# Kernel tuning notes

Hardware: AMD Instinct MI355X
Metric: run time of the kernel (lower is better)

## Reference

```python
import jax, jax.numpy as jnp
import numpy as np

B, ISIZE, HSIZE = 256, 256, 512
CLIPVAL = 2.0

def _linear(x, W, b):
    # torch nn.Linear: y = x @ W.T + b, W is [out, in]
    return x @ W.T + b

def setup_inputs() -> dict:
    key = jax.random.key(0)
    ks = jax.random.split(key, 24)
    d = {}
    d['inputs'] = jax.random.normal(ks[0], (B, ISIZE), jnp.float32)
    d['h0'] = jax.random.normal(ks[1], (B, HSIZE), jnp.float32) * 0.1
    d['c0'] = jax.random.normal(ks[2], (B, HSIZE), jnp.float32) * 0.1
    d['hebb'] = jax.random.normal(ks[3], (B, HSIZE, HSIZE), jnp.float32) * 0.01
    d['w'] = 0.02 * jax.random.uniform(ks[4], (HSIZE, HSIZE), jnp.float32) - 0.01
    d['alpha'] = 0.0001 * jax.random.uniform(ks[5], (1, 1, HSIZE), jnp.float32)
    scale_h = 1.0 / np.sqrt(HSIZE)
    scale_i = 1.0 / np.sqrt(ISIZE)
    d['h2f_w'] = jax.random.uniform(ks[6], (HSIZE, HSIZE), jnp.float32, -scale_h, scale_h)
    d['h2f_b'] = jax.random.uniform(ks[7], (HSIZE,), jnp.float32, -scale_h, scale_h)
    d['h2i_w'] = jax.random.uniform(ks[8], (HSIZE, HSIZE), jnp.float32, -scale_h, scale_h)
    d['h2i_b'] = jax.random.uniform(ks[9], (HSIZE,), jnp.float32, -scale_h, scale_h)
    d['h2opt_w'] = jax.random.uniform(ks[10], (HSIZE, HSIZE), jnp.float32, -scale_h, scale_h)
    d['h2opt_b'] = jax.random.uniform(ks[11], (HSIZE,), jnp.float32, -scale_h, scale_h)
    d['x2f_w'] = jax.random.uniform(ks[12], (HSIZE, ISIZE), jnp.float32, -scale_i, scale_i)
    d['x2f_b'] = jax.random.uniform(ks[13], (HSIZE,), jnp.float32, -scale_i, scale_i)
    d['x2i_w'] = jax.random.uniform(ks[14], (HSIZE, ISIZE), jnp.float32, -scale_i, scale_i)
    d['x2i_b'] = jax.random.uniform(ks[15], (HSIZE,), jnp.float32, -scale_i, scale_i)
    d['x2opt_w'] = jax.random.uniform(ks[16], (HSIZE, ISIZE), jnp.float32, -scale_i, scale_i)
    d['x2opt_b'] = jax.random.uniform(ks[17], (HSIZE,), jnp.float32, -scale_i, scale_i)
    d['x2c_w'] = jax.random.uniform(ks[18], (HSIZE, ISIZE), jnp.float32, -scale_i, scale_i)
    d['x2c_b'] = jax.random.uniform(ks[19], (HSIZE,), jnp.float32, -scale_i, scale_i)
    d['h2mod_w'] = jax.random.uniform(ks[20], (1, HSIZE), jnp.float32, -scale_h, scale_h)
    d['h2mod_b'] = jax.random.uniform(ks[21], (1,), jnp.float32, -scale_h, scale_h)
    d['modfanout_w'] = jax.random.uniform(ks[22], (HSIZE, 1), jnp.float32, -1.0, 1.0)
    d['modfanout_b'] = jax.random.uniform(ks[23], (HSIZE,), jnp.float32, -1.0, 1.0)
    return d

def reference(inputs, h0, c0, hebb, w, alpha,
              h2f_w, h2f_b, h2i_w, h2i_b, h2opt_w, h2opt_b,
              x2f_w, x2f_b, x2i_w, x2i_b, x2opt_w, x2opt_b, x2c_w, x2c_b,
              h2mod_w, h2mod_b, modfanout_w, modfanout_b):
    # gates
    fgt = jax.nn.sigmoid(_linear(inputs, x2f_w, x2f_b) + _linear(h0, h2f_w, h2f_b))
    ipt = jax.nn.sigmoid(_linear(inputs, x2i_w, x2i_b) + _linear(h0, h2i_w, h2i_b))
    opt = jax.nn.sigmoid(_linear(inputs, x2opt_w, x2opt_b) + _linear(h0, h2opt_w, h2opt_b))
    # plastic recurrent matmul: h [B,h] x (w + alpha*hebb) [B,h,h]
    M = w[None, :, :] + alpha * hebb  # [B, h, h]
    h2coutput = jnp.einsum('bh,bhk->bk', h0, M)
    inputstocell = jnp.tanh(_linear(inputs, x2c_w, x2c_b) + h2coutput)
    cell = fgt * c0 + ipt * inputstocell
    hactiv = opt * jnp.tanh(cell)
    # Hebbian outer product (hebboutput='i2c')
    deltahebb = h0[:, :, None] * inputstocell[:, None, :]  # [B, h, h]
    # modulation: modultype='modplasth2mod', modulout='fanout'
    m = jnp.tanh(_linear(hactiv, h2mod_w, h2mod_b))  # [B, 1]
    fan = m[:, 0][:, None] * modfanout_w[:, 0][None, :] + modfanout_b[None, :]  # [B, h]
    myeta = fan[:, None, :]  # [B, 1, h]
    # cliptype='clip'
    hebb_new = jnp.clip(hebb + myeta * deltahebb, -CLIPVAL, CLIPVAL)
    return hactiv, cell, hebb_new
```

## Files before the change

### kernel.cpp

```cpp
#include <hip/hip_runtime.h>
#include <math.h>

#define BATCH 256
#define ISZ 256
#define H 512
#define BH (BATCH * H)
#define CLIPV 2.0f

__device__ __forceinline__ float sigmoidf_(float x) { return 1.0f / (1.0f + expf(-x)); }

#define BT 64
#define KT 32
#define LDSP (BT + 4)

__global__ __launch_bounds__(256) void small_gemms(
    const float* __restrict__ x, const float* __restrict__ h0,
    const float* __restrict__ x2f_w, const float* __restrict__ x2f_b,
    const float* __restrict__ h2f_w, const float* __restrict__ h2f_b,
    const float* __restrict__ x2i_w, const float* __restrict__ x2i_b,
    const float* __restrict__ h2i_w, const float* __restrict__ h2i_b,
    const float* __restrict__ x2o_w, const float* __restrict__ x2o_b,
    const float* __restrict__ h2o_w, const float* __restrict__ h2o_b,
    const float* __restrict__ x2c_w, const float* __restrict__ x2c_b,
    const float* __restrict__ w,
    float* __restrict__ pre)
{
  __shared__ __align__(16) float As[KT][LDSP];
  __shared__ __align__(16) float Bs[KT][LDSP];
  const int z  = blockIdx.z;
  const int n0 = blockIdx.x * BT;
  const int m0 = blockIdx.y * BT;
  const int t  = threadIdx.x;
  const int tx = t & 15, ty = t >> 4;

  float acc[4][4] = {{0.0f}};

  const float* Aseg[2]; const float* Bseg[2];
  int ldaS[2], KS[2]; int nseg; bool kmajor = true;
  const float* xb = nullptr; const float* hbias = nullptr;

  if (z < 3) {
    const float* xw; const float* hw_;
    if (z == 0)      { xw = x2f_w; xb = x2f_b; hw_ = h2f_w; hbias = h2f_b; }
    else if (z == 1) { xw = x2i_w; xb = x2i_b; hw_ = h2i_w; hbias = h2i_b; }
    else             { xw = x2o_w; xb = x2o_b; hw_ = h2o_w; hbias = h2o_b; }
    Aseg[0] = x;  ldaS[0] = ISZ; Bseg[0] = xw;  KS[0] = ISZ;
    Aseg[1] = h0; ldaS[1] = H;   Bseg[1] = hw_; KS[1] = H;
    nseg = 2;
  } else if (z == 3) {
    Aseg[0] = x; ldaS[0] = ISZ; Bseg[0] = x2c_w; KS[0] = ISZ; xb = x2c_b;
    nseg = 1;
  } else {
    Aseg[0] = h0; ldaS[0] = H; Bseg[0] = w; KS[0] = H;
    nseg = 1; kmajor = false;
  }

  for (int s = 0; s < nseg; ++s) {
    const float* A  = Aseg[s];
    const float* Bm = Bseg[s];
    const int lda = ldaS[s];
    const int K   = KS[s];
    for (int kk0 = 0; kk0 < K; kk0 += KT) {
      #pragma unroll
      for (int i = 0; i < 8; ++i) {
        int l = i * 256 + t;
        int j = l & 31, r = l >> 5;
        As[j][r] = A[(size_t)(m0 + r) * lda + kk0 + j];
      }
      if (kmajor) {
        #pragma unroll
        for (int i = 0; i < 8; ++i) {
          int l = i * 256 + t;
          int j = l & 31, n = l >> 5;
          Bs[j][n] = Bm[(size_t)(n0 + n) * K + kk0 + j];
        }
      } else {
        #pragma unroll
        for (int i = 0; i < 8; ++i) {
          int l = i * 256 + t;
          int n = l & 63, j = l >> 6;
          Bs[j][n] = Bm[(size_t)(kk0 + j) * H + n0 + n];
        }
      }
      __syncthreads();
      #pragma unroll
      for (int j = 0; j < KT; ++j) {
        float4 a  = *(const float4*)&As[j][ty * 4];
        float4 bv = *(const float4*)&Bs[j][tx * 4];
        float av[4] = {a.x, a.y, a.z, a.w};
        float bw[4] = {bv.x, bv.y, bv.z, bv.w};
        #pragma unroll
        for (int r = 0; r < 4; ++r)
          #pragma unroll
          for (int c = 0; c < 4; ++c)
            acc[r][c] += av[r] * bw[c];
      }
      __syncthreads();
    }
  }

  float bias[4];
  #pragma unroll
  for (int c = 0; c < 4; ++c) {
    int n = n0 + tx * 4 + c;
    float bv = 0.0f;
    if (z < 3)       bv = xb[n] + hbias[n];
    else if (z == 3) bv = xb[n];
    bias[c] = bv;
  }
  float* outc = pre + (size_t)z * BH;
  #pragma unroll
  for (int r = 0; r < 4; ++r) {
    int m = m0 + ty * 4 + r;
    float4 o;
    o.x = acc[r][0] + bias[0];
    o.y = acc[r][1] + bias[1];
    o.z = acc[r][2] + bias[2];
    o.w = acc[r][3] + bias[3];
    *(float4*)&outc[(size_t)m * H + n0 + tx * 4] = o;
  }
}

__global__ __launch_bounds__(128) void einsum_partial(
    const float* __restrict__ h0, const float* __restrict__ hebb,
    float* __restrict__ hbpart)
{
  const int b    = blockIdx.x;
  const int hseg = blockIdx.y;
  const int t    = threadIdx.x;
  __shared__ float h0s[64];
  if (t < 64) h0s[t] = h0[b * H + hseg * 64 + t];
  __syncthreads();

  const float4* hb4 = (const float4*)(hebb + ((size_t)b * H + (size_t)hseg * 64) * H);
  float4 acc = {0.f, 0.f, 0.f, 0.f};
  #pragma unroll 8
  for (int h = 0; h < 64; ++h) {
    float4 v = hb4[(size_t)h * 128 + t];
    float s = h0s[h];
    acc.x += s * v.x; acc.y += s * v.y; acc.z += s * v.z; acc.w += s * v.w;
  }
  ((float4*)(hbpart + ((size_t)(b * 8 + hseg)) * H))[t] = acc;
}

__global__ __launch_bounds__(256) void fuse_gates(
    const float* __restrict__ pre, const float* __restrict__ hbpart,
    const float* __restrict__ c0, const float* __restrict__ alpha,
    float* __restrict__ out, float* __restrict__ itc)
{
  const int idx = blockIdx.x * 256 + threadIdx.x;
  const int k = idx & (H - 1);
  const int b = idx >> 9;
  float hb = 0.0f;
  #pragma unroll
  for (int s = 0; s < 8; ++s) hb += hbpart[((size_t)(b * 8 + s)) * H + k];
  float h2c  = pre[(size_t)4 * BH + idx] + alpha[k] * hb;
  float itcv = tanhf(pre[(size_t)3 * BH + idx] + h2c);
  float f = sigmoidf_(pre[(size_t)0 * BH + idx]);
  float i = sigmoidf_(pre[(size_t)1 * BH + idx]);
  float o = sigmoidf_(pre[(size_t)2 * BH + idx]);
  float cell = f * c0[idx] + i * itcv;
  float ha = o * tanhf(cell);
  out[idx] = ha;
  out[BH + idx] = cell;
  itc[idx] = itcv;
}

__global__ __launch_bounds__(256) void mod_eta(
    const float* __restrict__ hactiv,
    const float* __restrict__ h2mod_w, const float* __restrict__ h2mod_b,
    const float* __restrict__ mfo_w, const float* __restrict__ mfo_b,
    const float* __restrict__ itc, float* __restrict__ eta)
{
  const int b = blockIdx.x, t = threadIdx.x;
  float s = hactiv[b * H + t] * h2mod_w[t] + hactiv[b * H + 256 + t] * h2mod_w[256 + t];
  #pragma unroll
  for (int off = 32; off > 0; off >>= 1) s += __shfl_down(s, off, 64);
  __shared__ float red[4];
  __shared__ float mm;
  if ((t & 63) == 0) red[t >> 6] = s;
  __syncthreads();
  if (t == 0) mm = tanhf(red[0] + red[1] + red[2] + red[3] + h2mod_b[0]);
  __syncthreads();
  float m = mm;
  #pragma unroll
  for (int kk = t; kk < H; kk += 256) {
    float fan = m * mfo_w[kk] + mfo_b[kk];
    eta[b * H + kk] = fan * itc[b * H + kk];
  }
}

__global__ __launch_bounds__(256) void hebb_update(
    const float* __restrict__ hebb, const float* __restrict__ h0,
    const float* __restrict__ eta, float* __restrict__ out)
{
  const size_t g = (size_t)blockIdx.x * 256 + threadIdx.x;
  float4 v = ((const float4*)hebb)[g];
  const int k4  = (int)(g & 127);
  const int row = (int)(g >> 7);
  const int b   = row >> 9;
  float4 e = ((const float4*)eta)[(b << 7) + k4];
  float s = h0[row];
  float4 r;
  r.x = fminf(fmaxf(v.x + s * e.x, -CLIPV), CLIPV);
  r.y = fminf(fmaxf(v.y + s * e.y, -CLIPV), CLIPV);
  r.z = fminf(fmaxf(v.z + s * e.z, -CLIPV), CLIPV);
  r.w = fminf(fmaxf(v.w + s * e.w, -CLIPV), CLIPV);
  ((float4*)out)[(size_t)(2 * BH / 4) + g] = r;
}

extern "C" void kernel_launch(void* const* d_in, const int* in_sizes, int n_in,
                              void* d_out, int out_size, void* d_ws, size_t ws_size,
                              hipStream_t stream) {
  const float* x       = (const float*)d_in[0];
  const float* h0      = (const float*)d_in[1];
  const float* c0      = (const float*)d_in[2];
  const float* hebb    = (const float*)d_in[3];
  const float* w       = (const float*)d_in[4];
  const float* alpha   = (const float*)d_in[5];
  const float* h2f_w   = (const float*)d_in[6];
  const float* h2f_b   = (const float*)d_in[7];
  const float* h2i_w   = (const float*)d_in[8];
  const float* h2i_b   = (const float*)d_in[9];
  const float* h2o_w   = (const float*)d_in[10];
  const float* h2o_b   = (const float*)d_in[11];
  const float* x2f_w   = (const float*)d_in[12];
  const float* x2f_b   = (const float*)d_in[13];
  const float* x2i_w   = (const float*)d_in[14];
  const float* x2i_b   = (const float*)d_in[15];
  const float* x2o_w   = (const float*)d_in[16];
  const float* x2o_b   = (const float*)d_in[17];
  const float* x2c_w   = (const float*)d_in[18];
  const float* x2c_b   = (const float*)d_in[19];
  const float* h2mod_w = (const float*)d_in[20];
  const float* h2mod_b = (const float*)d_in[21];
  const float* mfo_w   = (const float*)d_in[22];
  const float* mfo_b   = (const float*)d_in[23];

  float* out = (float*)d_out;
  float* ws  = (float*)d_ws;

  float* pre    = ws;
  float* hbpart = pre + (size_t)5 * BH;
  float* itc    = hbpart + (size_t)BATCH * 8 * H;
  float* eta    = itc + BH;

  small_gemms<<<dim3(8, 4, 5), 256, 0, stream>>>(
      x, h0, x2f_w, x2f_b, h2f_w, h2f_b, x2i_w, x2i_b, h2i_w, h2i_b,
      x2o_w, x2o_b, h2o_w, h2o_b, x2c_w, x2c_b, w, pre);

  einsum_partial<<<dim3(BATCH, 8), 128, 0, stream>>>(h0, hebb, hbpart);

  fuse_gates<<<BH / 256, 256, 0, stream>>>(pre, hbpart, c0, alpha, out, itc);

  mod_eta<<<BATCH, 256, 0, stream>>>(out, h2mod_w, h2mod_b, mfo_w, mfo_b, itc, eta);

  hebb_update<<<(BH * H / 4) / 256, 256, 0, stream>>>(hebb, h0, eta, out);
}
```

Measured before the change: 673.4 us.

## Merge GEMMs with einsum, fuse gates with modulation, reverse hebb update order

The small GEMMs and the hebb einsum partial reductions now run in one launch, with block ranges selecting the role. Each einsum block uses 256 threads split into two halves and combines them through LDS. The gate kernel and the modulation/eta kernel are merged so the itc intermediate no longer goes through global memory. The hebb update walks blocks in reverse order, so the tail of hebb that was read last by the einsum may still be in cache, and it uses nontemporal loads and stores for the large streaming traffic. Together these cut launches and intermediate traffic, at the risk of load imbalance in the mixed-role kernel.

```diff
diff --git a/kernel.cpp b/kernel.cpp
--- a/kernel.cpp
+++ b/kernel.cpp
@@ -7,13 +7,19 @@
 #define BH (BATCH * H)
 #define CLIPV 2.0f
 
+typedef float f4_t __attribute__((ext_vector_type(4)));
+
 __device__ __forceinline__ float sigmoidf_(float x) { return 1.0f / (1.0f + expf(-x)); }
+__device__ __forceinline__ f4_t nt_load4(const f4_t* p) { return __builtin_nontemporal_load(p); }
+__device__ __forceinline__ void nt_store4(f4_t* p, f4_t v) { __builtin_nontemporal_store(v, p); }
 
 #define BT 64
 #define KT 32
 #define LDSP (BT + 4)
-
-__global__ __launch_bounds__(256) void small_gemms(
+#define NGEMM 160
+#define NEIN  2048
+
+__global__ __launch_bounds__(256) void gemms_einsum(
     const float* __restrict__ x, const float* __restrict__ h0,
     const float* __restrict__ x2f_w, const float* __restrict__ x2f_b,
     const float* __restrict__ h2f_w, const float* __restrict__ h2f_b,
@@ -23,14 +29,47 @@
     const float* __restrict__ h2o_w, const float* __restrict__ h2o_b,
     const float* __restrict__ x2c_w, const float* __restrict__ x2c_b,
     const float* __restrict__ w,
-    float* __restrict__ pre)
+    const float* __restrict__ hebb,
+    float* __restrict__ pre, float* __restrict__ hbpart)
 {
   __shared__ __align__(16) float As[KT][LDSP];
   __shared__ __align__(16) float Bs[KT][LDSP];
-  const int z  = blockIdx.z;
-  const int n0 = blockIdx.x * BT;
-  const int m0 = blockIdx.y * BT;
-  const int t  = threadIdx.x;
+  __shared__ float h0s[64];
+  __shared__ f4_t redv[128];
+
+  const int bid = blockIdx.x;
+  const int t   = threadIdx.x;
+
+  if (bid >= NGEMM) {
+    const int e    = bid - NGEMM;
+    const int b    = e >> 3;
+    const int hseg = e & 7;
+    const int col  = t & 127;
+    const int half = t >> 7;
+    if (t < 64) h0s[t] = h0[b * H + hseg * 64 + t];
+    __syncthreads();
+    const f4_t* hb4 = (const f4_t*)hebb +
+        (size_t)(b * H + hseg * 64 + half * 32) * (H / 4);
+    f4_t acc = {0.f, 0.f, 0.f, 0.f};
+    #pragma unroll 8
+    for (int h = 0; h < 32; ++h) {
+      f4_t v = hb4[(size_t)h * 128 + col];
+      float s = h0s[half * 32 + h];
+      acc += s * v;
+    }
+    if (half == 1) redv[col] = acc;
+    __syncthreads();
+    if (half == 0) {
+      acc += redv[col];
+      ((f4_t*)hbpart)[(size_t)(b * 8 + hseg) * 128 + col] = acc;
+    }
+    return;
+  }
+
+  const int z   = bid >> 5;
+  const int rem = bid & 31;
+  const int n0  = (rem & 7) * BT;
+  const int m0  = (rem >> 3) * BT;
   const int tx = t & 15, ty = t >> 4;
 
   float acc[4][4] = {{0.0f}};
@@ -121,59 +160,34 @@
   }
 }
 
-__global__ __launch_bounds__(128) void einsum_partial(
-    const float* __restrict__ h0, const float* __restrict__ hebb,
-    float* __restrict__ hbpart)
-{
-  const int b    = blockIdx.x;
-  const int hseg = blockIdx.y;
-  const int t    = threadIdx.x;
-  __shared__ float h0s[64];
-  if (t < 64) h0s[t] = h0[b * H + hseg * 64 + t];
-  __syncthreads();
-
-  const float4* hb4 = (const float4*)(hebb + ((size_t)b * H + (size_t)hseg * 64) * H);
-  float4 acc = {0.f, 0.f, 0.f, 0.f};
-  #pragma unroll 8
-  for (int h = 0; h < 64; ++h) {
-    float4 v = hb4[(size_t)h * 128 + t];
-    float s = h0s[h];
-    acc.x += s * v.x; acc.y += s * v.y; acc.z += s * v.z; acc.w += s * v.w;
-  }
-  ((float4*)(hbpart + ((size_t)(b * 8 + hseg)) * H))[t] = acc;
-}
-
-__global__ __launch_bounds__(256) void fuse_gates(
+__global__ __launch_bounds__(256) void fuse_mod(
     const float* __restrict__ pre, const float* __restrict__ hbpart,
     const float* __restrict__ c0, const float* __restrict__ alpha,
-    float* __restrict__ out, float* __restrict__ itc)
-{
-  const int idx = blockIdx.x * 256 + threadIdx.x;
-  const int k = idx & (H - 1);
-  const int b = idx >> 9;
-  float hb = 0.0f;
-  #pragma unroll
-  for (int s = 0; s < 8; ++s) hb += hbpart[((size_t)(b * 8 + s)) * H + k];
-  float h2c  = pre[(size_t)4 * BH + idx] + alpha[k] * hb;
-  float itcv = tanhf(pre[(size_t)3 * BH + idx] + h2c);
-  float f = sigmoidf_(pre[(size_t)0 * BH + idx]);
-  float i = sigmoidf_(pre[(size_t)1 * BH + idx]);
-  float o = sigmoidf_(pre[(size_t)2 * BH + idx]);
-  float cell = f * c0[idx] + i * itcv;
-  float ha = o * tanhf(cell);
-  out[idx] = ha;
-  out[BH + idx] = cell;
-  itc[idx] = itcv;
-}
-
-__global__ __launch_bounds__(256) void mod_eta(
-    const float* __restrict__ hactiv,
     const float* __restrict__ h2mod_w, const float* __restrict__ h2mod_b,
     const float* __restrict__ mfo_w, const float* __restrict__ mfo_b,
-    const float* __restrict__ itc, float* __restrict__ eta)
+    float* __restrict__ out, float* __restrict__ eta)
 {
   const int b = blockIdx.x, t = threadIdx.x;
-  float s = hactiv[b * H + t] * h2mod_w[t] + hactiv[b * H + 256 + t] * h2mod_w[256 + t];
+  float ha[2], itcv[2];
+  #pragma unroll
+  for (int u = 0; u < 2; ++u) {
+    const int k   = t + u * 256;
+    const int idx = b * H + k;
+    float hb = 0.0f;
+    #pragma unroll
+    for (int s = 0; s < 8; ++s) hb += hbpart[(size_t)(b * 8 + s) * H + k];
+    float h2c = pre[(size_t)4 * BH + idx] + alpha[k] * hb;
+    float it  = tanhf(pre[(size_t)3 * BH + idx] + h2c);
+    float f = sigmoidf_(pre[idx]);
+    float i = sigmoidf_(pre[(size_t)BH + idx]);
+    float o = sigmoidf_(pre[(size_t)2 * BH + idx]);
+    float cell = f * c0[idx] + i * it;
+    float h = o * tanhf(cell);
+    out[idx] = h;
+    out[BH + idx] = cell;
+    ha[u] = h; itcv[u] = it;
+  }
+  float s = ha[0] * h2mod_w[t] + ha[1] * h2mod_w[t + 256];
   #pragma unroll
   for (int off = 32; off > 0; off >>= 1) s += __shfl_down(s, off, 64);
   __shared__ float red[4];
@@ -184,9 +198,9 @@
   __syncthreads();
   float m = mm;
   #pragma unroll
-  for (int kk = t; kk < H; kk += 256) {
-    float fan = m * mfo_w[kk] + mfo_b[kk];
-    eta[b * H + kk] = fan * itc[b * H + kk];
+  for (int u = 0; u < 2; ++u) {
+    const int k = t + u * 256;
+    eta[b * H + k] = (m * mfo_w[k] + mfo_b[k]) * itcv[u];
   }
 }
 
@@ -194,19 +208,19 @@
     const float* __restrict__ hebb, const float* __restrict__ h0,
     const float* __restrict__ eta, float* __restrict__ out)
 {
-  const size_t g = (size_t)blockIdx.x * 256 + threadIdx.x;
-  float4 v = ((const float4*)hebb)[g];
+  const size_t g = (size_t)(gridDim.x - 1 - blockIdx.x) * 256 + threadIdx.x;
+  f4_t v = nt_load4((const f4_t*)hebb + g);
   const int k4  = (int)(g & 127);
   const int row = (int)(g >> 7);
   const int b   = row >> 9;
-  float4 e = ((const float4*)eta)[(b << 7) + k4];
+  f4_t e = ((const f4_t*)eta)[(b << 7) + k4];
   float s = h0[row];
-  float4 r;
+  f4_t r;
   r.x = fminf(fmaxf(v.x + s * e.x, -CLIPV), CLIPV);
   r.y = fminf(fmaxf(v.y + s * e.y, -CLIPV), CLIPV);
   r.z = fminf(fmaxf(v.z + s * e.z, -CLIPV), CLIPV);
   r.w = fminf(fmaxf(v.w + s * e.w, -CLIPV), CLIPV);
-  ((float4*)out)[(size_t)(2 * BH / 4) + g] = r;
+  nt_store4((f4_t*)out + (size_t)(2 * BH / 4) + g, r);
 }
 
 extern "C" void kernel_launch(void* const* d_in, const int* in_sizes, int n_in,
@@ -242,18 +256,14 @@
 
   float* pre    = ws;
   float* hbpart = pre + (size_t)5 * BH;
-  float* itc    = hbpart + (size_t)BATCH * 8 * H;
-  float* eta    = itc + BH;
-
-  small_gemms<<<dim3(8, 4, 5), 256, 0, stream>>>(
+  float* eta    = hbpart + (size_t)BATCH * 8 * H;
+
+  gemms_einsum<<<NGEMM + NEIN, 256, 0, stream>>>(
       x, h0, x2f_w, x2f_b, h2f_w, h2f_b, x2i_w, x2i_b, h2i_w, h2i_b,
-      x2o_w, x2o_b, h2o_w, h2o_b, x2c_w, x2c_b, w, pre);
-
-  einsum_partial<<<dim3(BATCH, 8), 128, 0, stream>>>(h0, hebb, hbpart);
-
-  fuse_gates<<<BH / 256, 256, 0, stream>>>(pre, hbpart, c0, alpha, out, itc);
-
-  mod_eta<<<BATCH, 256, 0, stream>>>(out, h2mod_w, h2mod_b, mfo_w, mfo_b, itc, eta);
-
-  hebb_update<<<(BH * H / 4) / 256, 256, 0, stream>>>(hebb, h0, eta, out);
-}
+      x2o_w, x2o_b, h2o_w, h2o_b, x2c_w, x2c_b, w, hebb, pre, hbpart);
+
+  fuse_mod<<<BATCH, 256, 0, stream>>>(
+      pre, hbpart, c0, alpha, h2mod_w, h2mod_b, mfo_w, mfo_b, out, eta);
+
+  hebb_update<<<(BH * (H / 4)) / 256, 256, 0, stream>>>(hebb, h0, eta, out);
+}
```

Measured after the change: 628.9 us. -6.6%, faster.
